# Kernel tuning notes

Hardware: AMD Instinct MI355X
Metric: run time of the kernel (lower is better)

The kernel has to match this reference:

```python
import jax, jax.numpy as jnp
import numpy as np
from functools import partial

EPS = 1e-5
TAU = 2.0
V_TH = 1.0
ALPHA = 4.0  # sigmoid surrogate sharpness (spikingjelly default)

@jax.custom_vjp
def heaviside(x):
    return (x >= 0.0).astype(x.dtype)

def _heaviside_fwd(x):
    return heaviside(x), x

def _heaviside_bwd(x, g):
    s = jax.nn.sigmoid(ALPHA * x)
    return (g * ALPHA * s * (1.0 - s),)

heaviside.defvjp(_heaviside_fwd, _heaviside_bwd)

def lif_multistep(x_seq):
    # x_seq: [T, ...]; LIF: v += (x - v)/tau; spike if v>=1; hard reset to 0 (detach_reset)
    def step(v, x):
        v = v + (x - v) / TAU
        spike = heaviside(v - V_TH)
        v = v * (1.0 - jax.lax.stop_gradient(spike))
        return v, spike
    _, spikes = jax.lax.scan(step, jnp.zeros_like(x_seq[0]), x_seq)
    return spikes

def bn_fold(g, b, m, v):
    scale = g * jax.lax.rsqrt(v + EPS)
    shift = b - m * scale
    return scale, shift

def setup_inputs() -> dict:
    key = jax.random.key(0)
    ks = jax.random.split(key, 11)
    T, B, C, H, W = 4, 32, 512, 32, 32
    HID, OUT = 64, 32
    return {
        "x": jax.random.normal(ks[0], (T, B, C, H, W), jnp.float32),
        "w1_w": jax.random.normal(ks[1], (HID, C), jnp.float32) * 0.05,
        "bn1_g": jax.random.uniform(ks[2], (HID,), jnp.float32, 0.5, 1.5),
        "bn1_b": jax.random.normal(ks[3], (HID,), jnp.float32) * 0.1,
        "bn1_m": jax.random.normal(ks[4], (HID,), jnp.float32) * 0.1,
        "bn1_v": jax.random.uniform(ks[5], (HID,), jnp.float32, 0.5, 1.5),
        "w2_w": jax.random.normal(ks[6], (OUT, HID), jnp.float32) * 0.1,
        "bn2_g": jax.random.uniform(ks[7], (OUT,), jnp.float32, 0.5, 1.5),
        "bn2_b": jax.random.normal(ks[8], (OUT,), jnp.float32) * 0.1,
        "bn2_m": jax.random.normal(ks[9], (OUT,), jnp.float32) * 0.1,
        "bn2_v": jax.random.uniform(ks[10], (OUT,), jnp.float32, 0.5, 1.5),
    }

def reference(x, w1_w, bn1_g, bn1_b, bn1_m, bn1_v, w2_w, bn2_g, bn2_b, bn2_m, bn2_v):
    T, B, C, H, W = x.shape
    N = H * W
    C_groups, L = 4, 8  # self.C=4, l=lidx+2=8; out_dim = C_groups*L
    xr = x.reshape(T, B, C, N)
    # conv1x1 + folded BN (inference)
    s1, sh1 = bn_fold(bn1_g, bn1_b, bn1_m, bn1_v)
    h = jnp.einsum('tbcn,oc->tbon', xr, w1_w)
    h = h * s1[:, None] + sh1[:, None]          # [T,B,HID,N]
    # spiking LIF temporal recurrence over T
    s = lif_multistep(h)                          # [T,B,HID,N]
    # conv1x1 + folded BN
    s2, sh2 = bn_fold(bn2_g, bn2_b, bn2_m, bn2_v)
    y = jnp.einsum('tbon,po->tbpn', s, w2_w)
    y = y * s2[:, None] + sh2[:, None]           # [T,B,OUT,N]
    # rearrange 'T B (C L) H W -> C T B L H W'
    dw = y.reshape(T, B, C_groups, L, H, W).transpose(2, 0, 1, 3, 4, 5)
    return dw
```

## Files before the change

### kernel.cpp

```cpp
#include <hip/hip_runtime.h>


#define T_   4
#define B_   32
#define C_   512
#define NPIX 1024
#define HID  64
#define OUTC 32
#define NT   64
#define CK   16
#define NCH  (C_ / CK)

typedef const __attribute__((address_space(1))) void* gas_t;
typedef __attribute__((address_space(3))) void* las_t;

__global__ __launch_bounds__(256, 2)
void snn_fused(const float* __restrict__ x,  const float* __restrict__ w1,
               const float* __restrict__ g1, const float* __restrict__ b1,
               const float* __restrict__ m1, const float* __restrict__ v1,
               const float* __restrict__ w2,
               const float* __restrict__ g2, const float* __restrict__ b2,
               const float* __restrict__ m2, const float* __restrict__ v2,
               float* __restrict__ out)
{
    __shared__ float xs[2][T_][CK][NT];
    __shared__ float w1s[2][HID][CK];
    __shared__ float w2s[HID][OUTC];
    __shared__ unsigned short spk[T_][4][NT];
    __shared__ float s2s[OUTC], sh2s[OUTC];

    const int tid = threadIdx.x;
    const int wv  = tid >> 6;
    const int ln  = tid & 63;
    const int b   = blockIdx.y;
    const int n0  = blockIdx.x * NT;

    {
        const int p  = tid & 31;
        const int ob = (tid >> 5) * 8;
        #pragma unroll
        for (int i = 0; i < 8; ++i)
            w2s[ob + i][p] = w2[p * HID + ob + i];
        if (tid < OUTC) {
            float sc  = g2[tid] / sqrtf(v2[tid] + 1e-5f);
            s2s[tid]  = sc;
            sh2s[tid] = b2[tid] - m2[tid] * sc;
        }
    }

    #define STAGE(ch, bf) do {                                                          \
        const int c0_ = (ch) * CK;                                                      \
        const float* gx_ = x + (((size_t)wv * B_ + b) * C_ + c0_) * NPIX + n0;          \
        _Pragma("unroll")                                                               \
        for (int j_ = 0; j_ < 4; ++j_) {                                                \
            const float* src_ = gx_ + (j_ * 4 + (ln >> 4)) * NPIX + ((ln & 15) << 2);   \
            __builtin_amdgcn_global_load_lds((gas_t)src_, (las_t)&xs[bf][wv][j_ * 4][0], 16, 0, 0); \
        }                                                                               \
        const float* sw_ = w1 + (size_t)(wv * 16 + (ln >> 2)) * C_ + c0_ + ((ln & 3) << 2); \
        __builtin_amdgcn_global_load_lds((gas_t)sw_, (las_t)&w1s[bf][wv * 16][0], 16, 0, 0); \
    } while (0)

    float h[T_][16];
    #pragma unroll
    for (int t = 0; t < T_; ++t)
        #pragma unroll
        for (int i = 0; i < 16; ++i) h[t][i] = 0.f;

    STAGE(0, 0);
    __syncthreads();

    int bf = 0;
    for (int ch = 0; ch < NCH; ++ch) {
        if (ch + 1 < NCH) STAGE(ch + 1, bf ^ 1);
        #pragma unroll
        for (int c4 = 0; c4 < CK; c4 += 4) {
            float xv[T_][4];
            #pragma unroll
            for (int t = 0; t < T_; ++t)
                #pragma unroll
                for (int cc = 0; cc < 4; ++cc)
                    xv[t][cc] = xs[bf][t][c4 + cc][ln];
            #pragma unroll
            for (int i = 0; i < 16; ++i) {
                const float4 wq = *(const float4*)&w1s[bf][wv * 16 + i][c4];
                const float wa[4] = {wq.x, wq.y, wq.z, wq.w};
                #pragma unroll
                for (int cc = 0; cc < 4; ++cc)
                    #pragma unroll
                    for (int t = 0; t < T_; ++t)
                        h[t][i] = fmaf(xv[t][cc], wa[cc], h[t][i]);
            }
        }
        __syncthreads();
        bf ^= 1;
    }

    {
        unsigned int msk[T_] = {0u, 0u, 0u, 0u};
        #pragma unroll
        for (int i = 0; i < 16; ++i) {
            const int o = wv * 16 + i;
            const float sc = g1[o] / sqrtf(v1[o] + 1e-5f);
            const float sh = b1[o] - m1[o] * sc;
            float v = 0.f;
            #pragma unroll
            for (int t = 0; t < T_; ++t) {
                const float hh = h[t][i] * sc + sh;
                v = v + (hh - v) * 0.5f;
                const bool sp = (v >= 1.0f);
                if (sp) msk[t] |= (1u << i);
                v = sp ? 0.f : v;
            }
        }
        #pragma unroll
        for (int t = 0; t < T_; ++t)
            spk[t][wv][ln] = (unsigned short)msk[t];
    }
    __syncthreads();

    {
        const int t = wv;
        const unsigned int mlo = (unsigned int)spk[t][0][ln] | ((unsigned int)spk[t][1][ln] << 16);
        const unsigned int mhi = (unsigned int)spk[t][2][ln] | ((unsigned int)spk[t][3][ln] << 16);

        float y[OUTC];
        #pragma unroll
        for (int p = 0; p < OUTC; ++p) y[p] = 0.f;

        #pragma unroll 4
        for (int o = 0; o < 32; ++o) {
            const float sp = (float)((mlo >> o) & 1u);
            #pragma unroll
            for (int p4 = 0; p4 < OUTC; p4 += 4) {
                const float4 wq = *(const float4*)&w2s[o][p4];
                y[p4 + 0] = fmaf(sp, wq.x, y[p4 + 0]);
                y[p4 + 1] = fmaf(sp, wq.y, y[p4 + 1]);
                y[p4 + 2] = fmaf(sp, wq.z, y[p4 + 2]);
                y[p4 + 3] = fmaf(sp, wq.w, y[p4 + 3]);
            }
        }
        #pragma unroll 4
        for (int o = 0; o < 32; ++o) {
            const float sp = (float)((mhi >> o) & 1u);
            #pragma unroll
            for (int p4 = 0; p4 < OUTC; p4 += 4) {
                const float4 wq = *(const float4*)&w2s[o + 32][p4];
                y[p4 + 0] = fmaf(sp, wq.x, y[p4 + 0]);
                y[p4 + 1] = fmaf(sp, wq.y, y[p4 + 1]);
                y[p4 + 2] = fmaf(sp, wq.z, y[p4 + 2]);
                y[p4 + 3] = fmaf(sp, wq.w, y[p4 + 3]);
            }
        }

        #pragma unroll
        for (int p = 0; p < OUTC; ++p) {
            const int cg = p >> 3, l = p & 7;
            const size_t idx = ((size_t)(((cg * T_ + t) * B_ + b) * 8 + l) << 10) + n0 + ln;
            out[idx] = y[p] * s2s[p] + sh2s[p];
        }
    }
    #undef STAGE
}

extern "C" void kernel_launch(void* const* d_in, const int* in_sizes, int n_in,
                              void* d_out, int out_size, void* d_ws, size_t ws_size,
                              hipStream_t stream)
{
    const float* x  = (const float*)d_in[0];
    const float* w1 = (const float*)d_in[1];
    const float* g1 = (const float*)d_in[2];
    const float* b1 = (const float*)d_in[3];
    const float* m1 = (const float*)d_in[4];
    const float* v1 = (const float*)d_in[5];
    const float* w2 = (const float*)d_in[6];
    const float* g2 = (const float*)d_in[7];
    const float* b2 = (const float*)d_in[8];
    const float* m2 = (const float*)d_in[9];
    const float* v2 = (const float*)d_in[10];

    dim3 grid(NPIX / NT, B_);
    snn_fused<<<grid, 256, 0, stream>>>(x, w1, g1, b1, m1, v1, w2, g2, b2, m2, v2,
                                        (float*)d_out);
}
```

Before: 562.2 us.

## Use packed FMA, scalar-load weights, double chunk size, pre-transpose w2

The GEMM accumulators become 2-wide float vectors so the compiler can emit packed FP32 FMA (v_pk_fma_f32). Because the wave index is made uniform with readfirstlane, w1 and w2 are read straight from global memory as wave-uniform scalar loads, and their LDS staging is removed. The channel chunk grows from 16 to 32. A separate tiny kernel transposes w2 into the workspace first. This trades LDS traffic and VALU instruction count for scalar-cache dependence and one extra launch, and it raises register pressure.

```diff
diff --git a/kernel.cpp b/kernel.cpp
--- a/kernel.cpp
+++ b/kernel.cpp
@@ -8,24 +8,31 @@
 #define HID  64
 #define OUTC 32
 #define NT   64
-#define CK   16
+#define CK   32
 #define NCH  (C_ / CK)
 
 typedef const __attribute__((address_space(1))) void* gas_t;
 typedef __attribute__((address_space(3))) void* las_t;
+typedef float v2f __attribute__((ext_vector_type(2)));
+
+__global__ void w2_transpose(const float* __restrict__ w2, float* __restrict__ wst)
+{
+    const int o = threadIdx.x;
+    #pragma unroll
+    for (int p = 0; p < OUTC; ++p)
+        wst[o * OUTC + p] = w2[p * HID + o];
+}
 
 __global__ __launch_bounds__(256, 2)
 void snn_fused(const float* __restrict__ x,  const float* __restrict__ w1,
                const float* __restrict__ g1, const float* __restrict__ b1,
                const float* __restrict__ m1, const float* __restrict__ v1,
-               const float* __restrict__ w2,
+               const float* __restrict__ wst,
                const float* __restrict__ g2, const float* __restrict__ b2,
                const float* __restrict__ m2, const float* __restrict__ v2,
                float* __restrict__ out)
 {
     __shared__ float xs[2][T_][CK][NT];
-    __shared__ float w1s[2][HID][CK];
-    __shared__ float w2s[HID][OUTC];
     __shared__ unsigned short spk[T_][4][NT];
     __shared__ float s2s[OUTC], sh2s[OUTC];
 
@@ -34,37 +41,29 @@
     const int ln  = tid & 63;
     const int b   = blockIdx.y;
     const int n0  = blockIdx.x * NT;
+    const int wvu = __builtin_amdgcn_readfirstlane(wv);
 
-    {
-        const int p  = tid & 31;
-        const int ob = (tid >> 5) * 8;
-        #pragma unroll
-        for (int i = 0; i < 8; ++i)
-            w2s[ob + i][p] = w2[p * HID + ob + i];
-        if (tid < OUTC) {
-            float sc  = g2[tid] / sqrtf(v2[tid] + 1e-5f);
-            s2s[tid]  = sc;
-            sh2s[tid] = b2[tid] - m2[tid] * sc;
-        }
+    if (tid < OUTC) {
+        float sc  = g2[tid] / sqrtf(v2[tid] + 1e-5f);
+        s2s[tid]  = sc;
+        sh2s[tid] = b2[tid] - m2[tid] * sc;
     }
 
     #define STAGE(ch, bf) do {                                                          \
         const int c0_ = (ch) * CK;                                                      \
         const float* gx_ = x + (((size_t)wv * B_ + b) * C_ + c0_) * NPIX + n0;          \
         _Pragma("unroll")                                                               \
-        for (int j_ = 0; j_ < 4; ++j_) {                                                \
+        for (int j_ = 0; j_ < 8; ++j_) {                                                \
             const float* src_ = gx_ + (j_ * 4 + (ln >> 4)) * NPIX + ((ln & 15) << 2);   \
             __builtin_amdgcn_global_load_lds((gas_t)src_, (las_t)&xs[bf][wv][j_ * 4][0], 16, 0, 0); \
         }                                                                               \
-        const float* sw_ = w1 + (size_t)(wv * 16 + (ln >> 2)) * C_ + c0_ + ((ln & 3) << 2); \
-        __builtin_amdgcn_global_load_lds((gas_t)sw_, (las_t)&w1s[bf][wv * 16][0], 16, 0, 0); \
     } while (0)
 
-    float h[T_][16];
+    v2f h01[16], h23[16];
     #pragma unroll
-    for (int t = 0; t < T_; ++t)
-        #pragma unroll
-        for (int i = 0; i < 16; ++i) h[t][i] = 0.f;
+    for (int i = 0; i < 16; ++i) { h01[i] = (v2f){0.f, 0.f}; h23[i] = (v2f){0.f, 0.f}; }
+
+    const float* w1u = w1 + (size_t)wvu * 16 * C_;
 
     STAGE(0, 0);
     __syncthreads();
@@ -72,23 +71,24 @@
     int bf = 0;
     for (int ch = 0; ch < NCH; ++ch) {
         if (ch + 1 < NCH) STAGE(ch + 1, bf ^ 1);
+        const float* wc = w1u + ch * CK;
         #pragma unroll
         for (int c4 = 0; c4 < CK; c4 += 4) {
-            float xv[T_][4];
+            v2f x01[4], x23[4];
             #pragma unroll
-            for (int t = 0; t < T_; ++t)
-                #pragma unroll
-                for (int cc = 0; cc < 4; ++cc)
-                    xv[t][cc] = xs[bf][t][c4 + cc][ln];
+            for (int cc = 0; cc < 4; ++cc) {
+                x01[cc] = (v2f){ xs[bf][0][c4 + cc][ln], xs[bf][1][c4 + cc][ln] };
+                x23[cc] = (v2f){ xs[bf][2][c4 + cc][ln], xs[bf][3][c4 + cc][ln] };
+            }
             #pragma unroll
             for (int i = 0; i < 16; ++i) {
-                const float4 wq = *(const float4*)&w1s[bf][wv * 16 + i][c4];
-                const float wa[4] = {wq.x, wq.y, wq.z, wq.w};
+                const float* wr = wc + i * C_ + c4;
                 #pragma unroll
-                for (int cc = 0; cc < 4; ++cc)
-                    #pragma unroll
-                    for (int t = 0; t < T_; ++t)
-                        h[t][i] = fmaf(xv[t][cc], wa[cc], h[t][i]);
+                for (int cc = 0; cc < 4; ++cc) {
+                    const v2f ws = { wr[cc], wr[cc] };
+                    h01[i] = __builtin_elementwise_fma(x01[cc], ws, h01[i]);
+                    h23[i] = __builtin_elementwise_fma(x23[cc], ws, h23[i]);
+                }
             }
         }
         __syncthreads();
@@ -99,14 +99,15 @@
         unsigned int msk[T_] = {0u, 0u, 0u, 0u};
         #pragma unroll
         for (int i = 0; i < 16; ++i) {
-            const int o = wv * 16 + i;
+            const int o = wvu * 16 + i;
             const float sc = g1[o] / sqrtf(v1[o] + 1e-5f);
             const float sh = b1[o] - m1[o] * sc;
+            const float hh[T_] = { h01[i].x, h01[i].y, h23[i].x, h23[i].y };
             float v = 0.f;
             #pragma unroll
             for (int t = 0; t < T_; ++t) {
-                const float hh = h[t][i] * sc + sh;
-                v = v + (hh - v) * 0.5f;
+                const float hb = hh[t] * sc + sh;
+                v = v + (hb - v) * 0.5f;
                 const bool sp = (v >= 1.0f);
                 if (sp) msk[t] |= (1u << i);
                 v = sp ? 0.f : v;
@@ -123,40 +124,39 @@
         const unsigned int mlo = (unsigned int)spk[t][0][ln] | ((unsigned int)spk[t][1][ln] << 16);
         const unsigned int mhi = (unsigned int)spk[t][2][ln] | ((unsigned int)spk[t][3][ln] << 16);
 
-        float y[OUTC];
+        v2f y2[16];
         #pragma unroll
-        for (int p = 0; p < OUTC; ++p) y[p] = 0.f;
+        for (int p2 = 0; p2 < 16; ++p2) y2[p2] = (v2f){0.f, 0.f};
 
-        #pragma unroll 4
+        #pragma unroll 8
         for (int o = 0; o < 32; ++o) {
             const float sp = (float)((mlo >> o) & 1u);
+            const v2f spv = { sp, sp };
+            const float* wr = wst + o * OUTC;
             #pragma unroll
-            for (int p4 = 0; p4 < OUTC; p4 += 4) {
-                const float4 wq = *(const float4*)&w2s[o][p4];
-                y[p4 + 0] = fmaf(sp, wq.x, y[p4 + 0]);
-                y[p4 + 1] = fmaf(sp, wq.y, y[p4 + 1]);
-                y[p4 + 2] = fmaf(sp, wq.z, y[p4 + 2]);
-                y[p4 + 3] = fmaf(sp, wq.w, y[p4 + 3]);
-            }
+            for (int p2 = 0; p2 < 16; ++p2)
+                y2[p2] = __builtin_elementwise_fma(spv, ((const v2f*)wr)[p2], y2[p2]);
         }
-        #pragma unroll 4
+        #pragma unroll 8
         for (int o = 0; o < 32; ++o) {
             const float sp = (float)((mhi >> o) & 1u);
+            const v2f spv = { sp, sp };
+            const float* wr = wst + (o + 32) * OUTC;
             #pragma unroll
-            for (int p4 = 0; p4 < OUTC; p4 += 4) {
-                const float4 wq = *(const float4*)&w2s[o + 32][p4];
-                y[p4 + 0] = fmaf(sp, wq.x, y[p4 + 0]);
-                y[p4 + 1] = fmaf(sp, wq.y, y[p4 + 1]);
-                y[p4 + 2] = fmaf(sp, wq.z, y[p4 + 2]);
-                y[p4 + 3] = fmaf(sp, wq.w, y[p4 + 3]);
-            }
+            for (int p2 = 0; p2 < 16; ++p2)
+                y2[p2] = __builtin_elementwise_fma(spv, ((const v2f*)wr)[p2], y2[p2]);
         }
 
         #pragma unroll
-        for (int p = 0; p < OUTC; ++p) {
-            const int cg = p >> 3, l = p & 7;
-            const size_t idx = ((size_t)(((cg * T_ + t) * B_ + b) * 8 + l) << 10) + n0 + ln;
-            out[idx] = y[p] * s2s[p] + sh2s[p];
+        for (int p2 = 0; p2 < 16; ++p2) {
+            const float yy[2] = { y2[p2].x, y2[p2].y };
+            #pragma unroll
+            for (int k = 0; k < 2; ++k) {
+                const int p  = p2 * 2 + k;
+                const int cg = p >> 3, l = p & 7;
+                const size_t idx = ((size_t)(((cg * T_ + t) * B_ + b) * 8 + l) << 10) + n0 + ln;
+                out[idx] = yy[k] * s2s[p] + sh2s[p];
+            }
         }
     }
     #undef STAGE
@@ -178,7 +178,10 @@
     const float* m2 = (const float*)d_in[9];
     const float* v2 = (const float*)d_in[10];
 
+    float* wst = (float*)d_ws;
+
+    w2_transpose<<<1, 64, 0, stream>>>(w2, wst);
     dim3 grid(NPIX / NT, B_);
-    snn_fused<<<grid, 256, 0, stream>>>(x, w1, g1, b1, m1, v1, w2, g2, b2, m2, v2,
+    snn_fused<<<grid, 256, 0, stream>>>(x, w1, g1, b1, m1, v1, wst, g2, b2, m2, v2,
                                         (float*)d_out);
 }
```

After: 540.8 us. -3.8%, faster.
